# Performance work log

Hardware: AMD Instinct MI355X
Metric: run time of the kernel (lower is better)

## Reference

```python
import jax, jax.numpy as jnp
import numpy as np

LAYERS = 2      # LightGCN propagation layers
LAMB = 0.5      # aux loss weight
REG = 1e-4      # embedding reg weight
N_AUX = 2       # len(behaviors) - 1


def setup_inputs() -> dict:
    key = jax.random.key(0)
    k = jax.random.split(key, 8)
    n_users, n_items, d = 100000, 50000, 32
    E = 1000000
    user_emb = (jax.random.normal(k[0], (n_users + 1, d), jnp.float32) * 0.1).at[0].set(0.0)
    item_emb = (jax.random.normal(k[1], (n_items + 1, d), jnp.float32) * 0.1).at[0].set(0.0)
    aux_u = jax.random.randint(k[2], (N_AUX, E), 1, n_users + 1)
    aux_i = jax.random.randint(k[3], (N_AUX, E), 1, n_items + 1)
    aux_edges = jnp.stack([aux_u, aux_i], axis=-1).astype(jnp.int32)
    tgt_u = jax.random.randint(k[4], (E,), 1, n_users + 1)
    tgt_i = jax.random.randint(k[5], (E,), 1, n_items + 1)
    target_edges = jnp.stack([tgt_u, tgt_i], axis=-1).astype(jnp.int32)
    # [B, 1+N_AUX, 3]: per row (user, pos_item, neg_item) for target then each aux behavior
    batch_data = jax.random.randint(k[6], (4096, 1 + N_AUX, 3), 1, n_items + 1).astype(jnp.int32)
    return {"user_emb": user_emb, "item_emb": item_emb, "batch_data": batch_data,
            "aux_edges": aux_edges, "target_edges": target_edges}


def _graph(edges, n_user_rows, N):
    """Symmetric-normalized bipartite LightGCN graph as directed COO (src, dst, w)."""
    u = edges[:, 0]
    v = edges[:, 1] + n_user_rows  # shift item ids into joint node space
    ones = jnp.ones(u.shape[0], jnp.float32)
    deg = jax.ops.segment_sum(ones, u, num_segments=N) + jax.ops.segment_sum(ones, v, num_segments=N)
    dinv = jnp.where(deg > 0, jax.lax.rsqrt(jnp.maximum(deg, 1.0)), 0.0)
    w = dinv[u] * dinv[v]
    src = jnp.concatenate([u, v])
    dst = jnp.concatenate([v, u])
    w2 = jnp.concatenate([w, w])
    return src, dst, w2


def _lightgcn(emb, src, dst, w, N):
    """L-layer LightGCN propagation, mean over layers 0..L."""
    acc = emb
    cur = emb
    for _ in range(LAYERS):
        cur = jax.ops.segment_sum(w[:, None] * cur[src], dst, num_segments=N)
        acc = acc + cur
    return acc / (LAYERS + 1)


def _prob(ue, ie, u, i):
    return jax.nn.relu(jnp.sum(ue[u] * ie[i], axis=-1))


def _bpr(p, n):
    return -jnp.mean(jax.nn.log_sigmoid(p - n))


def reference(user_emb, item_emb, batch_data, aux_edges, target_edges):
    Nu = user_emb.shape[0]
    N = Nu + item_emb.shape[0]
    all_emb = jnp.concatenate([user_emb, item_emb], axis=0)
    tgt_g = _graph(target_edges, Nu, N)

    user, p_item, n_item = batch_data[:, 0, 0], batch_data[:, 0, 1], batch_data[:, 0, 2]
    aux_user, aux_p, aux_n = batch_data[:, 1:, 0], batch_data[:, 1:, 1], batch_data[:, 1:, 2]

    cps, cns, dps, dns, aps, ans, aux_losses = [], [], [], [], [], [], []
    for idx in range(N_AUX):
        # combine graph = aux behavior edges union target edges
        comb_edges = jnp.concatenate([aux_edges[idx], target_edges], axis=0)
        ce = _lightgcn(all_emb, *_graph(comb_edges, Nu, N), N)
        cu, ci = ce[:Nu], ce[Nu:]
        cps.append(_prob(cu, ci, user, p_item))
        cns.append(_prob(cu, ci, user, n_item))

        ae = _lightgcn(all_emb, *_graph(aux_edges[idx], Nu, N), N)
        au, ai = ae[:Nu], ae[Nu:]
        aps.append(_prob(au, ai, user, p_item))
        ans.append(_prob(au, ai, user, n_item))

        # condition: propagate aux embeddings through the target graph
        de = _lightgcn(ae, *tgt_g, N)
        du, di = de[:Nu], de[Nu:]
        dps.append(_prob(du, di, user, p_item))
        dns.append(_prob(du, di, user, n_item))

        ps = jnp.sum(au[aux_user[:, idx]] * ai[aux_p[:, idx]], axis=-1)
        ns = jnp.sum(au[aux_user[:, idx]] * ai[aux_n[:, idx]], axis=-1)
        aux_losses.append(_bpr(ps, ns))

    aux_loss = jnp.mean(jnp.stack(aux_losses))

    def front_door(cond, comb, aux):
        return jnp.sum(cond * jnp.sum(comb * aux, axis=0), axis=0)

    p_scores = front_door(jnp.stack(dps), jnp.stack(cps), jnp.stack(aps))
    n_scores = front_door(jnp.stack(dns), jnp.stack(cns), jnp.stack(ans))
    rec_loss = _bpr(p_scores, n_scores)
    emb_loss = (jnp.linalg.norm(user_emb) + jnp.linalg.norm(item_emb)) / item_emb.shape[0]
    return rec_loss + LAMB * aux_loss + REG * emb_loss
```

## Files before the change

### kernel.cpp

```cpp
#include <hip/hip_runtime.h>
#include <math.h>

#define D 32
#define ROWU 16
#define NBK 1024
#define BSHIFT 8
#define TILE_H 16384
#define TILE_BIN 2048
#define BCAP 7680

typedef unsigned int u32;
typedef unsigned short u16;

__device__ __forceinline__ float logsigf(float x) {
  return fminf(x, 0.f) - log1pf(expf(-fabsf(x)));
}

__device__ __forceinline__ float lo16(u32 u) { return __uint_as_float(u << 16); }
__device__ __forceinline__ float hi16(u32 u) { return __uint_as_float(u & 0xFFFF0000u); }
__device__ __forceinline__ u32 pk2(float a, float b) {
  u32 ua = __float_as_uint(a), ub = __float_as_uint(b);
  u32 ra = (ua + 0x7FFFu + ((ua >> 16) & 1u)) >> 16;
  u32 rb = (ub + 0x7FFFu + ((ub >> 16) & 1u)) >> 16;
  return (ra & 0xFFFFu) | (rb << 16);
}
__device__ __forceinline__ float bfat(const u16* __restrict__ p, size_t off) {
  return __uint_as_float(((u32)p[off]) << 16);
}
__device__ __forceinline__ void accum8(float* a, float w, uint4 x) {
  a[0] += w * lo16(x.x); a[1] += w * hi16(x.x);
  a[2] += w * lo16(x.y); a[3] += w * hi16(x.y);
  a[4] += w * lo16(x.z); a[5] += w * hi16(x.z);
  a[6] += w * lo16(x.w); a[7] += w * hi16(x.w);
}
__device__ __forceinline__ uint4 pack8(const float* a, float w) {
  return make_uint4(pk2(w * a[0], w * a[1]), pk2(w * a[2], w * a[3]),
                    pk2(w * a[4], w * a[5]), pk2(w * a[6], w * a[7]));
}


__global__ void hist_kernel(const int2* __restrict__ tgt, const int2* __restrict__ aux,
                            int E, int Nu, int BPS, int* __restrict__ bcur) {
  __shared__ int lh[NBK];
  int seg = blockIdx.x / BPS;
  int blk = blockIdx.x - seg * BPS;
  const int2* edges = (seg == 0) ? tgt : aux + (size_t)(seg - 1) * E;
  for (int b = threadIdx.x; b < NBK; b += 256) lh[b] = 0;
  __syncthreads();
  int e0 = blk * TILE_H;
  for (int k = threadIdx.x; k < TILE_H; k += 256) {
    int e = e0 + k;
    if (e < E) {
      int2 ed = edges[e];
      atomicAdd(&lh[ed.x >> BSHIFT], 1);
      atomicAdd(&lh[(ed.y + Nu) >> BSHIFT], 1);
    }
  }
  __syncthreads();
  for (int b = threadIdx.x; b < NBK; b += 256)
    if (lh[b]) atomicAdd(&bcur[seg * NBK + b], lh[b]);
}

__global__ void bscan_kernel(int* __restrict__ bcur) {
  int* b = bcur + blockIdx.x * NBK;
  int lane = threadIdx.x;
  int carry = 0;
  for (int base = 0; base < NBK; base += 64) {
    int i = base + lane;
    int v = b[i];
    int s = v;
    #pragma unroll
    for (int o = 1; o < 64; o <<= 1) {
      int t = __shfl_up(s, o);
      if (lane >= o) s += t;
    }
    b[i] = carry + s - v;
    carry += __shfl(s, 63);
  }
}

__global__ void bin_kernel(const int2* __restrict__ tgt, const int2* __restrict__ aux,
                           int E, int Nu, int BPS, int* __restrict__ bcur,
                           int* __restrict__ binned) {
  __shared__ int stage[2 * TILE_BIN];
  __shared__ int lh[NBK];
  __shared__ int loff[NBK];
  __shared__ int gb[NBK];
  __shared__ int wred[4];
  __shared__ int stot;
  int seg = blockIdx.x / BPS;
  int blk = blockIdx.x - seg * BPS;
  const int2* edges = (seg == 0) ? tgt : aux + (size_t)(seg - 1) * E;
  int* out = binned + (size_t)seg * 2 * E;
  int tid = threadIdx.x;
  for (int b = tid; b < NBK; b += 256) lh[b] = 0;
  __syncthreads();
  int e0 = blk * TILE_BIN;
  int pkv[16];
  int pb[16];
  int pr[16];
  #pragma unroll
  for (int it = 0; it < 8; ++it) {
    int e = e0 + tid + it * 256;
    bool ok = e < E;
    int2 ed = ok ? edges[e] : make_int2(0, -Nu);
    int u = ed.x, v = ed.y + Nu;
    int b1 = u >> BSHIFT, b2 = v >> BSHIFT;
    pkv[2 * it] = ((u & 255) << 18) | v;
    pb[2 * it] = b1;
    pr[2 * it] = ok ? atomicAdd(&lh[b1], 1) : 0;
    pkv[2 * it + 1] = ((v & 255) << 18) | u;
    pb[2 * it + 1] = b2;
    pr[2 * it + 1] = ok ? atomicAdd(&lh[b2], 1) : 0;
  }
  __syncthreads();
  int lane = tid & 63, wid = tid >> 6;
  int b4 = tid * 4;
  int v0 = lh[b4], v1 = lh[b4 + 1], v2 = lh[b4 + 2], v3 = lh[b4 + 3];
  int tsum = v0 + v1 + v2 + v3;
  int incl = tsum;
  #pragma unroll
  for (int o = 1; o < 64; o <<= 1) {
    int t = __shfl_up(incl, o);
    if (lane >= o) incl += t;
  }
  if (lane == 63) wred[wid] = incl;
  __syncthreads();
  int wbase = 0;
  for (int w = 0; w < wid; ++w) wbase += wred[w];
  int excl = wbase + incl - tsum;
  loff[b4] = excl;
  loff[b4 + 1] = excl + v0;
  loff[b4 + 2] = excl + v0 + v1;
  loff[b4 + 3] = excl + v0 + v1 + v2;
  if (tid == 255) stot = excl + tsum;
  #pragma unroll
  for (int j = 0; j < 4; ++j) {
    int b = b4 + j;
    int c = lh[b];
    gb[b] = c ? atomicAdd(&bcur[seg * NBK + b], c) : 0;
  }
  __syncthreads();
  #pragma unroll
  for (int it = 0; it < 16; ++it) {
    int e = e0 + tid + (it >> 1) * 256;
    if (e < E) stage[loff[pb[it]] + pr[it]] = pkv[it];
  }
  __syncthreads();
  int tot = stot;
  for (int k = tid; k < tot; k += 256) {
    int lo = 0, hi = NBK;
    while (lo < hi) {
      int mid = (lo + hi) >> 1;
      if (loff[mid] <= k) lo = mid + 1; else hi = mid;
    }
    int b = lo - 1;
    out[gb[b] + (k - loff[b])] = stage[k];
  }
}

__global__ void bucket_csr_kernel(const int* __restrict__ binned,
                                  const int* __restrict__ bend, int E2, int N, int NBKe,
                                  int* __restrict__ deg3, int* __restrict__ rp3,
                                  int* __restrict__ col_all) {
  __shared__ int ent[BCAP];
  __shared__ int cnt[256];
  __shared__ int off[256];
  __shared__ int wred[4];
  int seg = blockIdx.x / NBKe;
  int bkt = blockIdx.x - seg * NBKe;
  int node0 = bkt << BSHIFT;
  const int* bc = bend + seg * NBK;
  int start = (bkt == 0) ? 0 : bc[bkt - 1];
  int end = bc[bkt];
  int cntE = end - start;
  const int* src = binned + (size_t)seg * E2 + start;
  bool inLds = (cntE <= BCAP);
  if (inLds)
    for (int k = threadIdx.x; k < cntE; k += 256) ent[k] = src[k];
  cnt[threadIdx.x] = 0;
  __syncthreads();
  for (int k = threadIdx.x; k < cntE; k += 256) {
    int en = inLds ? ent[k] : src[k];
    atomicAdd(&cnt[en >> 18], 1);
  }
  __syncthreads();
  int lane = threadIdx.x & 63, wid = threadIdx.x >> 6;
  int v = cnt[threadIdx.x];
  int incl = v;
  #pragma unroll
  for (int o = 1; o < 64; o <<= 1) {
    int t = __shfl_up(incl, o);
    if (lane >= o) incl += t;
  }
  if (lane == 63) wred[wid] = incl;
  __syncthreads();
  int wbase = 0;
  for (int w = 0; w < wid; ++w) wbase += wred[w];
  off[threadIdx.x] = wbase + incl - v;
  int node = node0 + (int)threadIdx.x;
  if (node < N) {
    deg3[(size_t)seg * N + node] = v;
    rp3[(size_t)seg * (N + 1) + node] = start + wbase + incl - v;
  }
  if (bkt == 0 && threadIdx.x == 0) rp3[(size_t)seg * (N + 1) + N] = E2;
  __syncthreads();
  cnt[threadIdx.x] = 0;
  __syncthreads();
  int* col = col_all + (size_t)seg * E2 + start;
  for (int k = threadIdx.x; k < cntE; k += 256) {
    int en = inLds ? ent[k] : src[k];
    int lb = en >> 18;
    int pos = atomicAdd(&cnt[lb], 1);
    col[off[lb] + pos] = en & 0x3FFFF;
  }
}

__global__ void dinv_all_kernel(const int* __restrict__ deg3, float* __restrict__ dinv5,
                                int N) {
  int n = blockIdx.x * blockDim.x + threadIdx.x;
  if (n >= N) return;
  int dt = deg3[n], d0 = deg3[N + n], d1 = deg3[2 * N + n];
  dinv5[n]         = dt ? rsqrtf((float)dt) : 0.f;
  dinv5[N + n]     = d0 ? rsqrtf((float)d0) : 0.f;
  dinv5[2 * N + n] = d1 ? rsqrtf((float)d1) : 0.f;
  int c0 = dt + d0, c1 = dt + d1;
  dinv5[3 * N + n] = c0 ? rsqrtf((float)c0) : 0.f;
  dinv5[4 * N + n] = c1 ? rsqrtf((float)c1) : 0.f;
}

__global__ void cvt_emb_kernel(const float2* __restrict__ ue, long nu2,
                               const float2* __restrict__ ie, long ni2,
                               u32* __restrict__ emb) {
  long i = (long)blockIdx.x * blockDim.x + threadIdx.x;
  if (i >= nu2 + ni2) return;
  float2 v = (i < nu2) ? ue[i] : ie[i - nu2];
  emb[i] = pk2(v.x, v.y);
}


__global__ void gather_fused_all_kernel(const int* __restrict__ rp3,
                                        const int* __restrict__ col_all,
                                        const float* __restrict__ dinv5,
                                        const uint4* __restrict__ emb,
                                        uint4* __restrict__ BaAll, uint4* __restrict__ BcAll,
                                        int N, int E2) {
  const int* rpA0 = rp3 + (size_t)1 * (N + 1);
  const int* rpA1 = rp3 + (size_t)2 * (N + 1);
  const int* colA0 = col_all + (size_t)1 * E2;
  const int* colA1 = col_all + (size_t)2 * E2;
  const float* dvA0 = dinv5 + (size_t)1 * N;
  const float* dvA1 = dinv5 + (size_t)2 * N;
  const float* dvC0 = dinv5 + (size_t)3 * N;
  const float* dvC1 = dinv5 + (size_t)4 * N;
  int t = blockIdx.x * blockDim.x + threadIdx.x;
  int n = t >> 2;
  if (n >= N) return;
  int lane = t & 3;
  float aA0[8] = {0, 0, 0, 0, 0, 0, 0, 0};
  float aA1[8] = {0, 0, 0, 0, 0, 0, 0, 0};
  float aC0[8] = {0, 0, 0, 0, 0, 0, 0, 0};
  float aC1[8] = {0, 0, 0, 0, 0, 0, 0, 0};
  int s = rpA0[n], e = rpA0[n + 1];
  int j = s;
  for (; j + 3 < e; j += 4) {
    int c0 = colA0[j], c1 = colA0[j + 1], c2 = colA0[j + 2], c3 = colA0[j + 3];
    uint4 x0 = emb[(size_t)c0 * 4 + lane];
    uint4 x1 = emb[(size_t)c1 * 4 + lane];
    uint4 x2 = emb[(size_t)c2 * 4 + lane];
    uint4 x3 = emb[(size_t)c3 * 4 + lane];
    accum8(aA0, dvA0[c0], x0); accum8(aC0, dvC0[c0], x0);
    accum8(aA0, dvA0[c1], x1); accum8(aC0, dvC0[c1], x1);
    accum8(aA0, dvA0[c2], x2); accum8(aC0, dvC0[c2], x2);
    accum8(aA0, dvA0[c3], x3); accum8(aC0, dvC0[c3], x3);
  }
  for (; j < e; ++j) {
    int c = colA0[j];
    uint4 x = emb[(size_t)c * 4 + lane];
    accum8(aA0, dvA0[c], x); accum8(aC0, dvC0[c], x);
  }
  s = rpA1[n]; e = rpA1[n + 1];
  j = s;
  for (; j + 3 < e; j += 4) {
    int c0 = colA1[j], c1 = colA1[j + 1], c2 = colA1[j + 2], c3 = colA1[j + 3];
    uint4 x0 = emb[(size_t)c0 * 4 + lane];
    uint4 x1 = emb[(size_t)c1 * 4 + lane];
    uint4 x2 = emb[(size_t)c2 * 4 + lane];
    uint4 x3 = emb[(size_t)c3 * 4 + lane];
    accum8(aA1, dvA1[c0], x0); accum8(aC1, dvC1[c0], x0);
    accum8(aA1, dvA1[c1], x1); accum8(aC1, dvC1[c1], x1);
    accum8(aA1, dvA1[c2], x2); accum8(aC1, dvC1[c2], x2);
    accum8(aA1, dvA1[c3], x3); accum8(aC1, dvC1[c3], x3);
  }
  for (; j < e; ++j) {
    int c = colA1[j];
    uint4 x = emb[(size_t)c * 4 + lane];
    accum8(aA1, dvA1[c], x); accum8(aC1, dvC1[c], x);
  }
  s = rp3[n]; e = rp3[n + 1];
  j = s;
  for (; j + 3 < e; j += 4) {
    int c0 = col_all[j], c1 = col_all[j + 1], c2 = col_all[j + 2], c3 = col_all[j + 3];
    uint4 x0 = emb[(size_t)c0 * 4 + lane];
    uint4 x1 = emb[(size_t)c1 * 4 + lane];
    uint4 x2 = emb[(size_t)c2 * 4 + lane];
    uint4 x3 = emb[(size_t)c3 * 4 + lane];
    accum8(aC0, dvC0[c0], x0); accum8(aC1, dvC1[c0], x0);
    accum8(aC0, dvC0[c1], x1); accum8(aC1, dvC1[c1], x1);
    accum8(aC0, dvC0[c2], x2); accum8(aC1, dvC1[c2], x2);
    accum8(aC0, dvC0[c3], x3); accum8(aC1, dvC1[c3], x3);
  }
  for (; j < e; ++j) {
    int c = col_all[j];
    uint4 x = emb[(size_t)c * 4 + lane];
    accum8(aC0, dvC0[c], x); accum8(aC1, dvC1[c], x);
  }
  size_t o = (size_t)n * 4 + lane;
  size_t rowN4 = (size_t)N * 4;
  BaAll[o] = pack8(aA0, dvA0[n]);
  BaAll[rowN4 + o] = pack8(aA1, dvA1[n]);
  BcAll[o] = pack8(aC0, dvC0[n]);
  BcAll[rowN4 + o] = pack8(aC1, dvC1[n]);
}

__global__ void gather_avg_kernel(const int* __restrict__ rp3, const int* __restrict__ col_all,
                                  const float* __restrict__ dinv5,
                                  const uint4* __restrict__ emb,
                                  const uint4* __restrict__ BaAll, uint4* __restrict__ AI,
                                  int N, int E2) {
  int idx = blockIdx.y;
  const int* rp = rp3 + (size_t)(1 + idx) * (N + 1);
  const int* col = col_all + (size_t)(1 + idx) * E2;
  const float* dv = dinv5 + (size_t)(1 + idx) * N;
  const uint4* cur = BaAll + (size_t)idx * N * 4;
  int t = blockIdx.x * blockDim.x + threadIdx.x;
  int n = t >> 2;
  if (n >= N) return;
  int lane = t & 3;
  float acc[8] = {0, 0, 0, 0, 0, 0, 0, 0};
  int s = rp[n], e = rp[n + 1];
  int j = s;
  for (; j + 3 < e; j += 4) {
    int c0 = col[j], c1 = col[j + 1], c2 = col[j + 2], c3 = col[j + 3];
    float w0 = dv[c0], w1 = dv[c1], w2 = dv[c2], w3 = dv[c3];
    uint4 x0 = cur[(size_t)c0 * 4 + lane];
    uint4 x1 = cur[(size_t)c1 * 4 + lane];
    uint4 x2 = cur[(size_t)c2 * 4 + lane];
    uint4 x3 = cur[(size_t)c3 * 4 + lane];
    accum8(acc, w0, x0);
    accum8(acc, w1, x1);
    accum8(acc, w2, x2);
    accum8(acc, w3, x3);
  }
  for (; j < e; ++j) {
    int c = col[j];
    float w = dv[c];
    uint4 x = cur[(size_t)c * 4 + lane];
    accum8(acc, w, x);
  }
  float wn = dv[n];
  uint4 e4 = emb[(size_t)n * 4 + lane];
  uint4 b4 = cur[(size_t)n * 4 + lane];
  float r[8];
  r[0] = (lo16(e4.x) + lo16(b4.x) + wn * acc[0]) * (1.f / 3.f);
  r[1] = (hi16(e4.x) + hi16(b4.x) + wn * acc[1]) * (1.f / 3.f);
  r[2] = (lo16(e4.y) + lo16(b4.y) + wn * acc[2]) * (1.f / 3.f);
  r[3] = (hi16(e4.y) + hi16(b4.y) + wn * acc[3]) * (1.f / 3.f);
  r[4] = (lo16(e4.z) + lo16(b4.z) + wn * acc[4]) * (1.f / 3.f);
  r[5] = (hi16(e4.z) + hi16(b4.z) + wn * acc[5]) * (1.f / 3.f);
  r[6] = (lo16(e4.w) + lo16(b4.w) + wn * acc[6]) * (1.f / 3.f);
  r[7] = (hi16(e4.w) + hi16(b4.w) + wn * acc[7]) * (1.f / 3.f);
  AI[(size_t)n * 8 + idx * 4 + lane] = pack8(r, 1.f);
}

__global__ void de_gather_kernel(const int* __restrict__ rp3, const int* __restrict__ col_all,
                                 const float* __restrict__ dinv5,
                                 const uint4* __restrict__ AI, uint4* __restrict__ DeI,
                                 int N) {
  int t = blockIdx.x * blockDim.x + threadIdx.x;
  int n = t >> 3;
  if (n >= N) return;
  int lane = t & 7;
  float acc[8] = {0, 0, 0, 0, 0, 0, 0, 0};
  int s = rp3[n], e = rp3[n + 1];
  int j = s;
  for (; j + 3 < e; j += 4) {
    int c0 = col_all[j], c1 = col_all[j + 1], c2 = col_all[j + 2], c3 = col_all[j + 3];
    float w0 = dinv5[c0], w1 = dinv5[c1], w2 = dinv5[c2], w3 = dinv5[c3];
    uint4 x0 = AI[(size_t)c0 * 8 + lane];
    uint4 x1 = AI[(size_t)c1 * 8 + lane];
    uint4 x2 = AI[(size_t)c2 * 8 + lane];
    uint4 x3 = AI[(size_t)c3 * 8 + lane];
    accum8(acc, w0, x0);
    accum8(acc, w1, x1);
    accum8(acc, w2, x2);
    accum8(acc, w3, x3);
  }
  for (; j < e; ++j) {
    int c = col_all[j];
    float w = dinv5[c];
    uint4 x = AI[(size_t)c * 8 + lane];
    accum8(acc, w, x);
  }
  DeI[(size_t)n * 8 + lane] = pack8(acc, dinv5[n]);
}


__device__ __forceinline__ float fdim2(const int* __restrict__ rpA, const int* __restrict__ colA,
                                       const int* __restrict__ rpT, const int* __restrict__ colT,
                                       const float* __restrict__ dv,
                                       const u16* __restrict__ base, const u16* __restrict__ L1,
                                       int r, int d) {
  float acc = 0.f;
  for (int j = rpA[r]; j < rpA[r + 1]; ++j) {
    int c = colA[j];
    acc += dv[c] * bfat(L1, (size_t)c * D + d);
  }
  for (int j = rpT[r]; j < rpT[r + 1]; ++j) {
    int c = colT[j];
    acc += dv[c] * bfat(L1, (size_t)c * D + d);
  }
  return (bfat(base, (size_t)r * D + d) + bfat(L1, (size_t)r * D + d) + dv[r] * acc) * (1.f / 3.f);
}

__device__ __forceinline__ float fdim1i(const int* __restrict__ rp, const int* __restrict__ col,
                                        const float* __restrict__ dv,
                                        const u16* __restrict__ base, const u16* __restrict__ L1,
                                        int r, int di) {
  float acc = 0.f;
  for (int j = rp[r]; j < rp[r + 1]; ++j) {
    int c = col[j];
    acc += dv[c] * bfat(L1, (size_t)c * 64 + di);
  }
  return (bfat(base, (size_t)r * 64 + di) + bfat(L1, (size_t)r * 64 + di) + dv[r] * acc) * (1.f / 3.f);
}

__global__ void ce_sparse_kernel(const int* __restrict__ rp3, const int* __restrict__ col_all,
                                 const float* __restrict__ dinv5,
                                 const u32* __restrict__ EMBu, const u32* __restrict__ BcAll,
                                 const int* __restrict__ batch, int Bsz, int Nu, int N, int E2,
                                 float* __restrict__ cps, float* __restrict__ cns) {
  int idx = blockIdx.y;
  const int* rpA = rp3 + (size_t)(1 + idx) * (N + 1);
  const int* colA = col_all + (size_t)(1 + idx) * E2;
  const float* dv = dinv5 + (size_t)(3 + idx) * N;
  const u16* base = (const u16*)EMBu;
  const u16* L1 = (const u16*)(BcAll + (size_t)idx * N * ROWU);
  float* outp = cps + (size_t)idx * Bsz;
  float* outn = cns + (size_t)idx * Bsz;
  int t = blockIdx.x * blockDim.x + threadIdx.x;
  int b = t >> 5, d = t & 31;
  if (b >= Bsz) return;
  int u = batch[b * 9 + 0];
  int p = batch[b * 9 + 1] + Nu;
  int n = batch[b * 9 + 2] + Nu;
  float uv = fdim2(rpA, colA, rp3, col_all, dv, base, L1, u, d);
  float pv = fdim2(rpA, colA, rp3, col_all, dv, base, L1, p, d);
  float nv = fdim2(rpA, colA, rp3, col_all, dv, base, L1, n, d);
  float sp = uv * pv, sn = uv * nv;
  #pragma unroll
  for (int o = 16; o > 0; o >>= 1) {
    sp += __shfl_down(sp, o, 32);
    sn += __shfl_down(sn, o, 32);
  }
  if (d == 0) {
    outp[b] = fmaxf(sp, 0.f);
    outn[b] = fmaxf(sn, 0.f);
  }
}

__global__ void de_sparse_kernel(const int* __restrict__ rp3, const int* __restrict__ col_all,
                                 const float* __restrict__ dinv5,
                                 const u32* __restrict__ AI, const u32* __restrict__ DeI,
                                 const int* __restrict__ batch, int Bsz, int Nu, int N,
                                 float* __restrict__ dps, float* __restrict__ dns) {
  int idx = blockIdx.y;
  const u16* base = (const u16*)AI;
  const u16* L1 = (const u16*)DeI;
  float* outp = dps + (size_t)idx * Bsz;
  float* outn = dns + (size_t)idx * Bsz;
  int t = blockIdx.x * blockDim.x + threadIdx.x;
  int b = t >> 5, d = t & 31;
  if (b >= Bsz) return;
  int di = idx * 32 + d;
  int u = batch[b * 9 + 0];
  int p = batch[b * 9 + 1] + Nu;
  int n = batch[b * 9 + 2] + Nu;
  float uv = fdim1i(rp3, col_all, dinv5, base, L1, u, di);
  float pv = fdim1i(rp3, col_all, dinv5, base, L1, p, di);
  float nv = fdim1i(rp3, col_all, dinv5, base, L1, n, di);
  float sp = uv * pv, sn = uv * nv;
  #pragma unroll
  for (int o = 16; o > 0; o >>= 1) {
    sp += __shfl_down(sp, o, 32);
    sn += __shfl_down(sn, o, 32);
  }
  if (d == 0) {
    outp[b] = fmaxf(sp, 0.f);
    outn[b] = fmaxf(sn, 0.f);
  }
}


__device__ __forceinline__ float dotrow(const u32* __restrict__ a, const u32* __restrict__ b) {
  float s = 0.f;
  #pragma unroll
  for (int k = 0; k < ROWU; ++k) {
    u32 x = a[k], y = b[k];
    s += lo16(x) * lo16(y) + hi16(x) * hi16(y);
  }
  return s;
}

__global__ void score_aux_kernel(const u32* __restrict__ AI, const int* __restrict__ batch,
                                 int Bsz, int Nu, int N, float* __restrict__ aps,
                                 float* __restrict__ ans_, float* __restrict__ accs) {
  int idx = blockIdx.y;
  const u32* A = AI + (size_t)idx * ROWU;
  float* outp = aps + (size_t)idx * Bsz;
  float* outn = ans_ + (size_t)idx * Bsz;
  int b = blockIdx.x * blockDim.x + threadIdx.x;
  float l = 0.f;
  if (b < Bsz) {
    int u = batch[b * 9 + 0];
    int p = batch[b * 9 + 1] + Nu;
    int n = batch[b * 9 + 2] + Nu;
    const u32* ur = A + (size_t)u * 32;
    outp[b] = fmaxf(dotrow(ur, A + (size_t)p * 32), 0.f);
    outn[b] = fmaxf(dotrow(ur, A + (size_t)n * 32), 0.f);
    const int* r = batch + b * 9 + 3 * (1 + idx);
    const u32* aur = A + (size_t)r[0] * 32;
    float ps = dotrow(aur, A + (size_t)(r[1] + Nu) * 32);
    float ns = dotrow(aur, A + (size_t)(r[2] + Nu) * 32);
    l = -logsigf(ps - ns);
  }
  for (int o = 32; o > 0; o >>= 1) l += __shfl_down(l, o);
  if ((threadIdx.x & 63) == 0) atomicAdd(&accs[idx], l);
}

__global__ void recloss_kernel(const float* __restrict__ cps, const float* __restrict__ cns,
                               const float* __restrict__ aps, const float* __restrict__ ans_,
                               const float* __restrict__ dps, const float* __restrict__ dns,
                               int Bsz, int NA, float* __restrict__ acc) {
  int b = blockIdx.x * blockDim.x + threadIdx.x;
  float l = 0.f;
  if (b < Bsz) {
    float dp = 0.f, dn = 0.f, cap = 0.f, can = 0.f;
    for (int i = 0; i < NA; ++i) {
      dp += dps[i * Bsz + b];
      dn += dns[i * Bsz + b];
      cap += cps[i * Bsz + b] * aps[i * Bsz + b];
      can += cns[i * Bsz + b] * ans_[i * Bsz + b];
    }
    l = -logsigf(dp * cap - dn * can);
  }
  for (int o = 32; o > 0; o >>= 1) l += __shfl_down(l, o);
  if ((threadIdx.x & 63) == 0) atomicAdd(acc, l);
}

__global__ void sumsq2_kernel(const float4* __restrict__ xu, int n4u,
                              const float4* __restrict__ xi, int n4i,
                              float* __restrict__ accU, float* __restrict__ accI) {
  __shared__ float redU[4], redI[4];
  int tid = threadIdx.x;
  int gid = blockIdx.x * blockDim.x + tid;
  int stride = gridDim.x * blockDim.x;
  float su = 0.f, si = 0.f;
  for (int i = gid; i < n4u; i += stride) {
    float4 v = xu[i];
    su += v.x * v.x + v.y * v.y + v.z * v.z + v.w * v.w;
  }
  for (int i = gid; i < n4i; i += stride) {
    float4 v = xi[i];
    si += v.x * v.x + v.y * v.y + v.z * v.z + v.w * v.w;
  }
  for (int o = 32; o > 0; o >>= 1) {
    su += __shfl_down(su, o);
    si += __shfl_down(si, o);
  }
  if ((tid & 63) == 0) { redU[tid >> 6] = su; redI[tid >> 6] = si; }
  __syncthreads();
  if (tid == 0) {
    atomicAdd(accU, redU[0] + redU[1] + redU[2] + redU[3]);
    atomicAdd(accI, redI[0] + redI[1] + redI[2] + redI[3]);
  }
}

__global__ void final_kernel(const float* __restrict__ accs, int Bsz, int NA, int NiRows,
                             float* __restrict__ out) {
  float rec = accs[NA] / (float)Bsz;
  float aux = 0.f;
  for (int i = 0; i < NA; ++i) aux += accs[i] / (float)Bsz;
  aux /= (float)NA;
  float embl = (sqrtf(accs[NA + 1]) + sqrtf(accs[NA + 2])) / (float)NiRows;
  out[0] = rec + 0.5f * aux + 1e-4f * embl;
}

extern "C" void kernel_launch(void* const* d_in, const int* in_sizes, int n_in,
                              void* d_out, int out_size, void* d_ws, size_t ws_size,
                              hipStream_t stream) {
  const float* user_emb = (const float*)d_in[0];
  const float* item_emb = (const float*)d_in[1];
  const int* batch = (const int*)d_in[2];
  const int* aux_edges = (const int*)d_in[3];
  const int* tgt_edges = (const int*)d_in[4];

  const int NuRows = in_sizes[0] / D;
  const int NiRows = in_sizes[1] / D;
  const int Bsz = in_sizes[2] / 9;
  const int E = in_sizes[4] / 2;
  const int NA = in_sizes[3] / (2 * E);
  const int N = NuRows + NiRows;
  const int E2 = 2 * E;
  const size_t rowH = (size_t)N * ROWU;
  const int BPS_H = (E + TILE_H - 1) / TILE_H;
  const int BPS_B = (E + TILE_BIN - 1) / TILE_BIN;
  const int NBKe = (N + (1 << BSHIFT) - 1) >> BSHIFT;

  u32* EMBu = (u32*)d_ws;
  u32* AI = EMBu + rowH;
  u32* BaAll = AI + 2 * rowH;
  u32* BcAll = BaAll + 2 * rowH;
  int* deg3 = (int*)(BcAll + 2 * rowH);
  float* dinv5 = (float*)(deg3 + 3 * (size_t)N);
  int* rp3 = (int*)(dinv5 + 5 * (size_t)N);
  int* bcur = rp3 + 3 * (size_t)(N + 1);
  int* col_all = bcur + 3 * (size_t)NBK;
  float* cps = (float*)(col_all + 3 * (size_t)E2);
  float* cns = cps + (size_t)NA * Bsz;
  float* aps = cns + (size_t)NA * Bsz;
  float* ans_ = aps + (size_t)NA * Bsz;
  float* dps = ans_ + (size_t)NA * Bsz;
  float* dns = dps + (size_t)NA * Bsz;
  float* accs = dns + (size_t)NA * Bsz;
  int* binned = (int*)AI;

  const int TB = 256;
  const int gN = (N + TB - 1) / TB;
  const int gN4 = (N * 4 + TB - 1) / TB;
  const int gN8 = (N * 8 + TB - 1) / TB;
  const int gB = (Bsz + TB - 1) / TB;
  const int gB32 = (Bsz * 32 + TB - 1) / TB;
  const long nu2 = (long)NuRows * ROWU;
  const long ni2 = (long)NiRows * ROWU;
  const int gCvt = (int)((nu2 + ni2 + TB - 1) / TB);

  cvt_emb_kernel<<<gCvt, TB, 0, stream>>>((const float2*)user_emb, nu2,
                                          (const float2*)item_emb, ni2, EMBu);

  hipMemsetAsync(bcur, 0, 3 * (size_t)NBK * sizeof(int), stream);
  hist_kernel<<<3 * BPS_H, TB, 0, stream>>>((const int2*)tgt_edges, (const int2*)aux_edges,
                                            E, NuRows, BPS_H, bcur);
  bscan_kernel<<<3, 64, 0, stream>>>(bcur);
  bin_kernel<<<3 * BPS_B, TB, 0, stream>>>((const int2*)tgt_edges, (const int2*)aux_edges,
                                           E, NuRows, BPS_B, bcur, binned);
  bucket_csr_kernel<<<3 * NBKe, TB, 0, stream>>>(binned, bcur, E2, N, NBKe,
                                                 deg3, rp3, col_all);
  dinv_all_kernel<<<gN, TB, 0, stream>>>(deg3, dinv5, N);

  hipMemsetAsync(accs, 0, (size_t)(NA + 3) * sizeof(float), stream);

  dim3 gridG(gN4, NA), gridB(gB, NA), gridS(gB32, NA);

  gather_fused_all_kernel<<<gN4, TB, 0, stream>>>(rp3, col_all, dinv5, (const uint4*)EMBu,
                                                  (uint4*)BaAll, (uint4*)BcAll, N, E2);
  gather_avg_kernel<<<gridG, TB, 0, stream>>>(rp3, col_all, dinv5, (const uint4*)EMBu,
                                              (const uint4*)BaAll, (uint4*)AI, N, E2);
  score_aux_kernel<<<gridB, TB, 0, stream>>>(AI, batch, Bsz, NuRows, N, aps, ans_, accs);
  ce_sparse_kernel<<<gridS, TB, 0, stream>>>(rp3, col_all, dinv5, EMBu, BcAll,
                                             batch, Bsz, NuRows, N, E2, cps, cns);
  de_gather_kernel<<<gN8, TB, 0, stream>>>(rp3, col_all, dinv5, (const uint4*)AI,
                                           (uint4*)BaAll, N);
  de_sparse_kernel<<<gridS, TB, 0, stream>>>(rp3, col_all, dinv5, AI, BaAll,
                                             batch, Bsz, NuRows, N, dps, dns);

  sumsq2_kernel<<<104, TB, 0, stream>>>((const float4*)user_emb,
                                        (int)((size_t)NuRows * D / 4),
                                        (const float4*)item_emb,
                                        (int)((size_t)NiRows * D / 4),
                                        accs + NA + 1, accs + NA + 2);
  recloss_kernel<<<gB, TB, 0, stream>>>(cps, cns, aps, ans_, dps, dns, Bsz, NA, accs + NA);
  final_kernel<<<1, 1, 0, stream>>>(accs, Bsz, NA, NiRows, (float*)d_out);
}
```

Baseline: 631.6 us.

## Pack neighbor index with fp16 edge weights in CSR, load edges cooperatively

CSR construction is split into a count pass and a scatter pass that runs after the degree normalization. Each CSR entry now stores the neighbor index together with two half-precision dinv weights, so the gather kernels no longer do random dinv lookups per edge. The gather loops also read four edges per quad with one coalesced load and broadcast them through shuffles. In exchange the edge array doubles in size, the extra kernel re-reads the binned data, and the weights lose precision by going to fp16.

```diff
diff --git a/kernel.cpp b/kernel.cpp
--- a/kernel.cpp
+++ b/kernel.cpp
@@ -1,4 +1,5 @@
 #include <hip/hip_runtime.h>
+#include <hip/hip_fp16.h>
 #include <math.h>
 
 #define D 32
@@ -7,7 +8,6 @@
 #define BSHIFT 8
 #define TILE_H 16384
 #define TILE_BIN 2048
-#define BCAP 7680
 
 typedef unsigned int u32;
 typedef unsigned short u16;
@@ -36,6 +36,16 @@
 __device__ __forceinline__ uint4 pack8(const float* a, float w) {
   return make_uint4(pk2(w * a[0], w * a[1]), pk2(w * a[2], w * a[3]),
                     pk2(w * a[4], w * a[5]), pk2(w * a[6], w * a[7]));
+}
+
+__device__ __forceinline__ int wpack(float a, float b) {
+  __half2 h = __floats2half2_rn(a, b);
+  return *reinterpret_cast<int*>(&h);
+}
+__device__ __forceinline__ float2 hun(int wb) {
+  __half2 h;
+  *reinterpret_cast<int*>(&h) = wb;
+  return __half22float2(h);
 }
 
 
@@ -159,13 +169,10 @@
   }
 }
 
-__global__ void bucket_csr_kernel(const int* __restrict__ binned,
-                                  const int* __restrict__ bend, int E2, int N, int NBKe,
-                                  int* __restrict__ deg3, int* __restrict__ rp3,
-                                  int* __restrict__ col_all) {
-  __shared__ int ent[BCAP];
+__global__ void csr_count_kernel(const int* __restrict__ binned,
+                                 const int* __restrict__ bend, int E2, int N, int NBKe,
+                                 int* __restrict__ deg3, int* __restrict__ rp3) {
   __shared__ int cnt[256];
-  __shared__ int off[256];
   __shared__ int wred[4];
   int seg = blockIdx.x / NBKe;
   int bkt = blockIdx.x - seg * NBKe;
@@ -175,15 +182,9 @@
   int end = bc[bkt];
   int cntE = end - start;
   const int* src = binned + (size_t)seg * E2 + start;
-  bool inLds = (cntE <= BCAP);
-  if (inLds)
-    for (int k = threadIdx.x; k < cntE; k += 256) ent[k] = src[k];
   cnt[threadIdx.x] = 0;
   __syncthreads();
-  for (int k = threadIdx.x; k < cntE; k += 256) {
-    int en = inLds ? ent[k] : src[k];
-    atomicAdd(&cnt[en >> 18], 1);
-  }
+  for (int k = threadIdx.x; k < cntE; k += 256) atomicAdd(&cnt[src[k] >> 18], 1);
   __syncthreads();
   int lane = threadIdx.x & 63, wid = threadIdx.x >> 6;
   int v = cnt[threadIdx.x];
@@ -197,23 +198,12 @@
   __syncthreads();
   int wbase = 0;
   for (int w = 0; w < wid; ++w) wbase += wred[w];
-  off[threadIdx.x] = wbase + incl - v;
   int node = node0 + (int)threadIdx.x;
   if (node < N) {
     deg3[(size_t)seg * N + node] = v;
     rp3[(size_t)seg * (N + 1) + node] = start + wbase + incl - v;
   }
   if (bkt == 0 && threadIdx.x == 0) rp3[(size_t)seg * (N + 1) + N] = E2;
-  __syncthreads();
-  cnt[threadIdx.x] = 0;
-  __syncthreads();
-  int* col = col_all + (size_t)seg * E2 + start;
-  for (int k = threadIdx.x; k < cntE; k += 256) {
-    int en = inLds ? ent[k] : src[k];
-    int lb = en >> 18;
-    int pos = atomicAdd(&cnt[lb], 1);
-    col[off[lb] + pos] = en & 0x3FFFF;
-  }
 }
 
 __global__ void dinv_all_kernel(const int* __restrict__ deg3, float* __restrict__ dinv5,
@@ -229,6 +219,38 @@
   dinv5[4 * N + n] = c1 ? rsqrtf((float)c1) : 0.f;
 }
 
+__global__ void csr_scatter_kernel(const int* __restrict__ binned,
+                                   const int* __restrict__ bend,
+                                   const int* __restrict__ rp3,
+                                   const float* __restrict__ dinv5,
+                                   int E2, int N, int NBKe,
+                                   int2* __restrict__ pk) {
+  __shared__ int cnt[256];
+  __shared__ int off[256];
+  int seg = blockIdx.x / NBKe;
+  int bkt = blockIdx.x - seg * NBKe;
+  int node0 = bkt << BSHIFT;
+  const int* bc = bend + seg * NBK;
+  int start = (bkt == 0) ? 0 : bc[bkt - 1];
+  int end = bc[bkt];
+  int cntE = end - start;
+  const int* src = binned + (size_t)seg * E2 + start;
+  int node = node0 + (int)threadIdx.x;
+  off[threadIdx.x] = (node < N) ? rp3[(size_t)seg * (N + 1) + node] : 0;
+  cnt[threadIdx.x] = 0;
+  const float* dvL = dinv5 + (size_t)(seg == 0 ? 3 : seg) * N;
+  const float* dvH = dinv5 + (size_t)(seg == 0 ? 4 : seg + 2) * N;
+  __syncthreads();
+  int2* out = pk + (size_t)seg * E2;
+  for (int k = threadIdx.x; k < cntE; k += 256) {
+    int en = src[k];
+    int lb = en >> 18;
+    int c = en & 0x3FFFF;
+    int pos = atomicAdd(&cnt[lb], 1);
+    out[off[lb] + pos] = make_int2(c, wpack(dvL[c], dvH[c]));
+  }
+}
+
 __global__ void cvt_emb_kernel(const float2* __restrict__ ue, long nu2,
                                const float2* __restrict__ ie, long ni2,
                                u32* __restrict__ emb) {
@@ -240,23 +262,25 @@
 
 
 __global__ void gather_fused_all_kernel(const int* __restrict__ rp3,
-                                        const int* __restrict__ col_all,
+                                        const int2* __restrict__ pk,
                                         const float* __restrict__ dinv5,
                                         const uint4* __restrict__ emb,
                                         uint4* __restrict__ BaAll, uint4* __restrict__ BcAll,
                                         int N, int E2) {
-  const int* rpA0 = rp3 + (size_t)1 * (N + 1);
-  const int* rpA1 = rp3 + (size_t)2 * (N + 1);
-  const int* colA0 = col_all + (size_t)1 * E2;
-  const int* colA1 = col_all + (size_t)2 * E2;
-  const float* dvA0 = dinv5 + (size_t)1 * N;
-  const float* dvA1 = dinv5 + (size_t)2 * N;
-  const float* dvC0 = dinv5 + (size_t)3 * N;
-  const float* dvC1 = dinv5 + (size_t)4 * N;
+  const int* rpA0 = rp3 + (size_t)(N + 1);
+  const int* rpA1 = rp3 + 2 * (size_t)(N + 1);
+  const int2* pT = pk;
+  const int2* pA0 = pk + (size_t)E2;
+  const int2* pA1 = pk + 2 * (size_t)E2;
+  const float* dvA0 = dinv5 + (size_t)N;
+  const float* dvA1 = dinv5 + 2 * (size_t)N;
+  const float* dvC0 = dinv5 + 3 * (size_t)N;
+  const float* dvC1 = dinv5 + 4 * (size_t)N;
   int t = blockIdx.x * blockDim.x + threadIdx.x;
   int n = t >> 2;
   if (n >= N) return;
   int lane = t & 3;
+  int qb = (threadIdx.x & 63) & 60;
   float aA0[8] = {0, 0, 0, 0, 0, 0, 0, 0};
   float aA1[8] = {0, 0, 0, 0, 0, 0, 0, 0};
   float aC0[8] = {0, 0, 0, 0, 0, 0, 0, 0};
@@ -264,56 +288,62 @@
   int s = rpA0[n], e = rpA0[n + 1];
   int j = s;
   for (; j + 3 < e; j += 4) {
-    int c0 = colA0[j], c1 = colA0[j + 1], c2 = colA0[j + 2], c3 = colA0[j + 3];
-    uint4 x0 = emb[(size_t)c0 * 4 + lane];
-    uint4 x1 = emb[(size_t)c1 * 4 + lane];
-    uint4 x2 = emb[(size_t)c2 * 4 + lane];
-    uint4 x3 = emb[(size_t)c3 * 4 + lane];
-    accum8(aA0, dvA0[c0], x0); accum8(aC0, dvC0[c0], x0);
-    accum8(aA0, dvA0[c1], x1); accum8(aC0, dvC0[c1], x1);
-    accum8(aA0, dvA0[c2], x2); accum8(aC0, dvC0[c2], x2);
-    accum8(aA0, dvA0[c3], x3); accum8(aC0, dvC0[c3], x3);
+    int2 en = pA0[j + lane];
+    #pragma unroll
+    for (int q = 0; q < 4; ++q) {
+      int c = __shfl(en.x, qb + q);
+      float2 w = hun(__shfl(en.y, qb + q));
+      uint4 x = emb[(size_t)c * 4 + lane];
+      accum8(aA0, w.x, x);
+      accum8(aC0, w.y, x);
+    }
   }
   for (; j < e; ++j) {
-    int c = colA0[j];
-    uint4 x = emb[(size_t)c * 4 + lane];
-    accum8(aA0, dvA0[c], x); accum8(aC0, dvC0[c], x);
+    int2 en = pA0[j];
+    float2 w = hun(en.y);
+    uint4 x = emb[(size_t)en.x * 4 + lane];
+    accum8(aA0, w.x, x);
+    accum8(aC0, w.y, x);
   }
   s = rpA1[n]; e = rpA1[n + 1];
   j = s;
   for (; j + 3 < e; j += 4) {
-    int c0 = colA1[j], c1 = colA1[j + 1], c2 = colA1[j + 2], c3 = colA1[j + 3];
-    uint4 x0 = emb[(size_t)c0 * 4 + lane];
-    uint4 x1 = emb[(size_t)c1 * 4 + lane];
-    uint4 x2 = emb[(size_t)c2 * 4 + lane];
-    uint4 x3 = emb[(size_t)c3 * 4 + lane];
-    accum8(aA1, dvA1[c0], x0); accum8(aC1, dvC1[c0], x0);
-    accum8(aA1, dvA1[c1], x1); accum8(aC1, dvC1[c1], x1);
-    accum8(aA1, dvA1[c2], x2); accum8(aC1, dvC1[c2], x2);
-    accum8(aA1, dvA1[c3], x3); accum8(aC1, dvC1[c3], x3);
+    int2 en = pA1[j + lane];
+    #pragma unroll
+    for (int q = 0; q < 4; ++q) {
+      int c = __shfl(en.x, qb + q);
+      float2 w = hun(__shfl(en.y, qb + q));
+      uint4 x = emb[(size_t)c * 4 + lane];
+      accum8(aA1, w.x, x);
+      accum8(aC1, w.y, x);
+    }
   }
   for (; j < e; ++j) {
-    int c = colA1[j];
-    uint4 x = emb[(size_t)c * 4 + lane];
-    accum8(aA1, dvA1[c], x); accum8(aC1, dvC1[c], x);
+    int2 en = pA1[j];
+    float2 w = hun(en.y);
+    uint4 x = emb[(size_t)en.x * 4 + lane];
+    accum8(aA1, w.x, x);
+    accum8(aC1, w.y, x);
   }
   s = rp3[n]; e = rp3[n + 1];
   j = s;
   for (; j + 3 < e; j += 4) {
-    int c0 = col_all[j], c1 = col_all[j + 1], c2 = col_all[j + 2], c3 = col_all[j + 3];
-    uint4 x0 = emb[(size_t)c0 * 4 + lane];
-    uint4 x1 = emb[(size_t)c1 * 4 + lane];
-    uint4 x2 = emb[(size_t)c2 * 4 + lane];
-    uint4 x3 = emb[(size_t)c3 * 4 + lane];
-    accum8(aC0, dvC0[c0], x0); accum8(aC1, dvC1[c0], x0);
-    accum8(aC0, dvC0[c1], x1); accum8(aC1, dvC1[c1], x1);
-    accum8(aC0, dvC0[c2], x2); accum8(aC1, dvC1[c2], x2);
-    accum8(aC0, dvC0[c3], x3); accum8(aC1, dvC1[c3], x3);
+    int2 en = pT[j + lane];
+    #pragma unroll
+    for (int q = 0; q < 4; ++q) {
+      int c = __shfl(en.x, qb + q);
+      float2 w = hun(__shfl(en.y, qb + q));
+      uint4 x = emb[(size_t)c * 4 + lane];
+      accum8(aC0, w.x, x);
+      accum8(aC1, w.y, x);
+    }
   }
   for (; j < e; ++j) {
-    int c = col_all[j];
-    uint4 x = emb[(size_t)c * 4 + lane];
-    accum8(aC0, dvC0[c], x); accum8(aC1, dvC1[c], x);
+    int2 en = pT[j];
+    float2 w = hun(en.y);
+    uint4 x = emb[(size_t)en.x * 4 + lane];
+    accum8(aC0, w.x, x);
+    accum8(aC1, w.y, x);
   }
   size_t o = (size_t)n * 4 + lane;
   size_t rowN4 = (size_t)N * 4;
@@ -323,40 +353,39 @@
   BcAll[rowN4 + o] = pack8(aC1, dvC1[n]);
 }
 
-__global__ void gather_avg_kernel(const int* __restrict__ rp3, const int* __restrict__ col_all,
+__global__ void gather_avg_kernel(const int* __restrict__ rp3, const int2* __restrict__ pk,
                                   const float* __restrict__ dinv5,
                                   const uint4* __restrict__ emb,
                                   const uint4* __restrict__ BaAll, uint4* __restrict__ AI,
                                   int N, int E2) {
   int idx = blockIdx.y;
   const int* rp = rp3 + (size_t)(1 + idx) * (N + 1);
-  const int* col = col_all + (size_t)(1 + idx) * E2;
+  const int2* pA = pk + (size_t)(1 + idx) * E2;
   const float* dv = dinv5 + (size_t)(1 + idx) * N;
   const uint4* cur = BaAll + (size_t)idx * N * 4;
   int t = blockIdx.x * blockDim.x + threadIdx.x;
   int n = t >> 2;
   if (n >= N) return;
   int lane = t & 3;
+  int qb = (threadIdx.x & 63) & 60;
   float acc[8] = {0, 0, 0, 0, 0, 0, 0, 0};
   int s = rp[n], e = rp[n + 1];
   int j = s;
   for (; j + 3 < e; j += 4) {
-    int c0 = col[j], c1 = col[j + 1], c2 = col[j + 2], c3 = col[j + 3];
-    float w0 = dv[c0], w1 = dv[c1], w2 = dv[c2], w3 = dv[c3];
-    uint4 x0 = cur[(size_t)c0 * 4 + lane];
-    uint4 x1 = cur[(size_t)c1 * 4 + lane];
-    uint4 x2 = cur[(size_t)c2 * 4 + lane];
-    uint4 x3 = cur[(size_t)c3 * 4 + lane];
-    accum8(acc, w0, x0);
-    accum8(acc, w1, x1);
-    accum8(acc, w2, x2);
-    accum8(acc, w3, x3);
+    int2 en = pA[j + lane];
+    #pragma unroll
+    for (int q = 0; q < 4; ++q) {
+      int c = __shfl(en.x, qb + q);
+      float2 w = hun(__shfl(en.y, qb + q));
+      uint4 x = cur[(size_t)c * 4 + lane];
+      accum8(acc, w.x, x);
+    }
   }
   for (; j < e; ++j) {
-    int c = col[j];
-    float w = dv[c];
-    uint4 x = cur[(size_t)c * 4 + lane];
-    accum8(acc, w, x);
+    int2 en = pA[j];
+    float2 w = hun(en.y);
+    uint4 x = cur[(size_t)en.x * 4 + lane];
+    accum8(acc, w.x, x);
   }
   float wn = dv[n];
   uint4 e4 = emb[(size_t)n * 4 + lane];
@@ -373,7 +402,7 @@
   AI[(size_t)n * 8 + idx * 4 + lane] = pack8(r, 1.f);
 }
 
-__global__ void de_gather_kernel(const int* __restrict__ rp3, const int* __restrict__ col_all,
+__global__ void de_gather_kernel(const int* __restrict__ rp3, const int2* __restrict__ pk,
                                  const float* __restrict__ dinv5,
                                  const uint4* __restrict__ AI, uint4* __restrict__ DeI,
                                  int N) {
@@ -381,68 +410,68 @@
   int n = t >> 3;
   if (n >= N) return;
   int lane = t & 7;
+  int gb = (threadIdx.x & 63) & 56;
   float acc[8] = {0, 0, 0, 0, 0, 0, 0, 0};
   int s = rp3[n], e = rp3[n + 1];
   int j = s;
   for (; j + 3 < e; j += 4) {
-    int c0 = col_all[j], c1 = col_all[j + 1], c2 = col_all[j + 2], c3 = col_all[j + 3];
-    float w0 = dinv5[c0], w1 = dinv5[c1], w2 = dinv5[c2], w3 = dinv5[c3];
-    uint4 x0 = AI[(size_t)c0 * 8 + lane];
-    uint4 x1 = AI[(size_t)c1 * 8 + lane];
-    uint4 x2 = AI[(size_t)c2 * 8 + lane];
-    uint4 x3 = AI[(size_t)c3 * 8 + lane];
-    accum8(acc, w0, x0);
-    accum8(acc, w1, x1);
-    accum8(acc, w2, x2);
-    accum8(acc, w3, x3);
+    int2 en = pk[j + (lane & 3)];
+    #pragma unroll
+    for (int q = 0; q < 4; ++q) {
+      int c = __shfl(en.x, gb + q);
+      float w = dinv5[c];
+      uint4 x = AI[(size_t)c * 8 + lane];
+      accum8(acc, w, x);
+    }
   }
   for (; j < e; ++j) {
-    int c = col_all[j];
-    float w = dinv5[c];
-    uint4 x = AI[(size_t)c * 8 + lane];
+    int2 en = pk[j];
+    float w = dinv5[en.x];
+    uint4 x = AI[(size_t)en.x * 8 + lane];
     accum8(acc, w, x);
   }
   DeI[(size_t)n * 8 + lane] = pack8(acc, dinv5[n]);
 }
 
 
-__device__ __forceinline__ float fdim2(const int* __restrict__ rpA, const int* __restrict__ colA,
-                                       const int* __restrict__ rpT, const int* __restrict__ colT,
-                                       const float* __restrict__ dv,
+__device__ __forceinline__ float fdim2(const int2* __restrict__ pkA, const int2* __restrict__ pkT,
+                                       const int* __restrict__ rpA, const int* __restrict__ rpT,
+                                       int idx, const float* __restrict__ dv,
                                        const u16* __restrict__ base, const u16* __restrict__ L1,
                                        int r, int d) {
   float acc = 0.f;
   for (int j = rpA[r]; j < rpA[r + 1]; ++j) {
-    int c = colA[j];
-    acc += dv[c] * bfat(L1, (size_t)c * D + d);
+    int2 en = pkA[j];
+    acc += hun(en.y).y * bfat(L1, (size_t)en.x * D + d);
   }
   for (int j = rpT[r]; j < rpT[r + 1]; ++j) {
-    int c = colT[j];
-    acc += dv[c] * bfat(L1, (size_t)c * D + d);
+    int2 en = pkT[j];
+    float2 w = hun(en.y);
+    acc += (idx ? w.y : w.x) * bfat(L1, (size_t)en.x * D + d);
   }
   return (bfat(base, (size_t)r * D + d) + bfat(L1, (size_t)r * D + d) + dv[r] * acc) * (1.f / 3.f);
 }
 
-__device__ __forceinline__ float fdim1i(const int* __restrict__ rp, const int* __restrict__ col,
+__device__ __forceinline__ float fdim1i(const int2* __restrict__ pkT, const int* __restrict__ rp,
                                         const float* __restrict__ dv,
                                         const u16* __restrict__ base, const u16* __restrict__ L1,
                                         int r, int di) {
   float acc = 0.f;
   for (int j = rp[r]; j < rp[r + 1]; ++j) {
-    int c = col[j];
-    acc += dv[c] * bfat(L1, (size_t)c * 64 + di);
+    int2 en = pkT[j];
+    acc += dv[en.x] * bfat(L1, (size_t)en.x * 64 + di);
   }
   return (bfat(base, (size_t)r * 64 + di) + bfat(L1, (size_t)r * 64 + di) + dv[r] * acc) * (1.f / 3.f);
 }
 
-__global__ void ce_sparse_kernel(const int* __restrict__ rp3, const int* __restrict__ col_all,
+__global__ void ce_sparse_kernel(const int* __restrict__ rp3, const int2* __restrict__ pk,
                                  const float* __restrict__ dinv5,
                                  const u32* __restrict__ EMBu, const u32* __restrict__ BcAll,
                                  const int* __restrict__ batch, int Bsz, int Nu, int N, int E2,
                                  float* __restrict__ cps, float* __restrict__ cns) {
   int idx = blockIdx.y;
   const int* rpA = rp3 + (size_t)(1 + idx) * (N + 1);
-  const int* colA = col_all + (size_t)(1 + idx) * E2;
+  const int2* pkA = pk + (size_t)(1 + idx) * E2;
   const float* dv = dinv5 + (size_t)(3 + idx) * N;
   const u16* base = (const u16*)EMBu;
   const u16* L1 = (const u16*)(BcAll + (size_t)idx * N * ROWU);
@@ -454,9 +483,9 @@
   int u = batch[b * 9 + 0];
   int p = batch[b * 9 + 1] + Nu;
   int n = batch[b * 9 + 2] + Nu;
-  float uv = fdim2(rpA, colA, rp3, col_all, dv, base, L1, u, d);
-  float pv = fdim2(rpA, colA, rp3, col_all, dv, base, L1, p, d);
-  float nv = fdim2(rpA, colA, rp3, col_all, dv, base, L1, n, d);
+  float uv = fdim2(pkA, pk, rpA, rp3, idx, dv, base, L1, u, d);
+  float pv = fdim2(pkA, pk, rpA, rp3, idx, dv, base, L1, p, d);
+  float nv = fdim2(pkA, pk, rpA, rp3, idx, dv, base, L1, n, d);
   float sp = uv * pv, sn = uv * nv;
   #pragma unroll
   for (int o = 16; o > 0; o >>= 1) {
@@ -469,7 +498,7 @@
   }
 }
 
-__global__ void de_sparse_kernel(const int* __restrict__ rp3, const int* __restrict__ col_all,
+__global__ void de_sparse_kernel(const int* __restrict__ rp3, const int2* __restrict__ pk,
                                  const float* __restrict__ dinv5,
                                  const u32* __restrict__ AI, const u32* __restrict__ DeI,
                                  const int* __restrict__ batch, int Bsz, int Nu, int N,
@@ -486,9 +515,9 @@
   int u = batch[b * 9 + 0];
   int p = batch[b * 9 + 1] + Nu;
   int n = batch[b * 9 + 2] + Nu;
-  float uv = fdim1i(rp3, col_all, dinv5, base, L1, u, di);
-  float pv = fdim1i(rp3, col_all, dinv5, base, L1, p, di);
-  float nv = fdim1i(rp3, col_all, dinv5, base, L1, n, di);
+  float uv = fdim1i(pk, rp3, dinv5, base, L1, u, di);
+  float pv = fdim1i(pk, rp3, dinv5, base, L1, p, di);
+  float nv = fdim1i(pk, rp3, dinv5, base, L1, n, di);
   float sp = uv * pv, sn = uv * nv;
   #pragma unroll
   for (int o = 16; o > 0; o >>= 1) {
@@ -625,8 +654,9 @@
   float* dinv5 = (float*)(deg3 + 3 * (size_t)N);
   int* rp3 = (int*)(dinv5 + 5 * (size_t)N);
   int* bcur = rp3 + 3 * (size_t)(N + 1);
-  int* col_all = bcur + 3 * (size_t)NBK;
-  float* cps = (float*)(col_all + 3 * (size_t)E2);
+  uintptr_t pka = ((uintptr_t)(bcur + 3 * (size_t)NBK) + 7) & ~(uintptr_t)7;
+  int2* pk = (int2*)pka;
+  float* cps = (float*)(pk + 3 * (size_t)E2);
   float* cns = cps + (size_t)NA * Bsz;
   float* aps = cns + (size_t)NA * Bsz;
   float* ans_ = aps + (size_t)NA * Bsz;
@@ -654,24 +684,24 @@
   bscan_kernel<<<3, 64, 0, stream>>>(bcur);
   bin_kernel<<<3 * BPS_B, TB, 0, stream>>>((const int2*)tgt_edges, (const int2*)aux_edges,
                                            E, NuRows, BPS_B, bcur, binned);
-  bucket_csr_kernel<<<3 * NBKe, TB, 0, stream>>>(binned, bcur, E2, N, NBKe,
-                                                 deg3, rp3, col_all);
+  csr_count_kernel<<<3 * NBKe, TB, 0, stream>>>(binned, bcur, E2, N, NBKe, deg3, rp3);
   dinv_all_kernel<<<gN, TB, 0, stream>>>(deg3, dinv5, N);
+  csr_scatter_kernel<<<3 * NBKe, TB, 0, stream>>>(binned, bcur, rp3, dinv5, E2, N, NBKe, pk);
 
   hipMemsetAsync(accs, 0, (size_t)(NA + 3) * sizeof(float), stream);
 
   dim3 gridG(gN4, NA), gridB(gB, NA), gridS(gB32, NA);
 
-  gather_fused_all_kernel<<<gN4, TB, 0, stream>>>(rp3, col_all, dinv5, (const uint4*)EMBu,
+  gather_fused_all_kernel<<<gN4, TB, 0, stream>>>(rp3, pk, dinv5, (const uint4*)EMBu,
                                                   (uint4*)BaAll, (uint4*)BcAll, N, E2);
-  gather_avg_kernel<<<gridG, TB, 0, stream>>>(rp3, col_all, dinv5, (const uint4*)EMBu,
+  gather_avg_kernel<<<gridG, TB, 0, stream>>>(rp3, pk, dinv5, (const uint4*)EMBu,
                                               (const uint4*)BaAll, (uint4*)AI, N, E2);
   score_aux_kernel<<<gridB, TB, 0, stream>>>(AI, batch, Bsz, NuRows, N, aps, ans_, accs);
-  ce_sparse_kernel<<<gridS, TB, 0, stream>>>(rp3, col_all, dinv5, EMBu, BcAll,
+  ce_sparse_kernel<<<gridS, TB, 0, stream>>>(rp3, pk, dinv5, EMBu, BcAll,
                                              batch, Bsz, NuRows, N, E2, cps, cns);
-  de_gather_kernel<<<gN8, TB, 0, stream>>>(rp3, col_all, dinv5, (const uint4*)AI,
+  de_gather_kernel<<<gN8, TB, 0, stream>>>(rp3, pk, dinv5, (const uint4*)AI,
                                            (uint4*)BaAll, N);
-  de_sparse_kernel<<<gridS, TB, 0, stream>>>(rp3, col_all, dinv5, AI, BaAll,
+  de_sparse_kernel<<<gridS, TB, 0, stream>>>(rp3, pk, dinv5, AI, (const u32*)BaAll,
                                              batch, Bsz, NuRows, N, dps, dns);
 
   sumsq2_kernel<<<104, TB, 0, stream>>>((const float4*)user_emb,
```

New measurement: 668.0 us. +5.8%, slower.
